# Optimization experiments

Hardware: AMD Instinct MI355X
Metric: run time of the kernel (lower is better)

## Reference

```python
import jax, jax.numpy as jnp
import numpy as np

T, G, D = 64, 1024, 128      # timesteps, detections per timestep, feature dim
N = T * G                    # total points; output rows = 3 + D = 131 cols


def setup_inputs() -> dict:
    key = jax.random.key(0)
    k1, k2 = jax.random.split(key)
    # time column: T distinct timestamps, G detections each (already time-sorted)
    times = jnp.repeat(jnp.arange(T, dtype=jnp.float32), G)
    xy = jax.random.uniform(k1, (N, 2), dtype=jnp.float32) * 128.0
    coor = jnp.concatenate([times[:, None], xy], axis=1)          # [N, 3]
    features = jax.random.normal(k2, (N, D), dtype=jnp.float32)   # [N, 128]
    return {"coor": coor, "features": features, "min_length": 8}


def _traverse(nxt):
    """Greedy chain building with a visited set (faithful to the torch loop).
    nxt[i] = precomputed best cosine match of point i in the next time group
    (-1 if i is in the last group). Returns (out_nodes, cid, clen):
      out_nodes[p] = node emitted at output slot p (all N slots filled),
      cid[p]       = chain id of slot p,
      clen[c]      = length of chain c.
    """
    def chain_cond(carry):
        visited, out, cid, p, cur, length, c = carry
        nx = nxt[cur]
        return (nx >= 0) & (~visited[nx])

    def chain_body(carry):
        visited, out, cid, p, cur, length, c = carry
        nx = nxt[cur]
        visited = visited.at[nx].set(True)
        out = out.at[p].set(nx)
        cid = cid.at[p].set(c)
        return (visited, out, cid, p + 1, nx, length + 1, c)

    def start_chain(st, start):
        visited, out, cid, clen, p, c = st
        visited = visited.at[start].set(True)
        out = out.at[p].set(start)
        cid = cid.at[p].set(c)
        carry = (visited, out, cid, p + 1, start, jnp.int32(1), c)
        visited, out, cid, p, cur, length, _ = jax.lax.while_loop(
            chain_cond, chain_body, carry)
        clen = clen.at[c].set(length)
        return (visited, out, cid, clen, p, c + 1)

    def body(start, st):
        start = jnp.int32(start)
        return jax.lax.cond(st[0][start], lambda s: s,
                            lambda s: start_chain(s, start), st)

    init = (jnp.zeros(N, bool),
            jnp.full(N, -1, jnp.int32),
            jnp.zeros(N, jnp.int32),
            jnp.zeros(N, jnp.int32),
            jnp.int32(0), jnp.int32(0))
    visited, out, cid, clen, p, c = jax.lax.fori_loop(0, N, body, init)
    return out, cid, clen


def reference(coor, features, min_length):
    # sort all points by time (stable; input is already time-sorted)
    order = jnp.argsort(coor[:, 0], stable=True)
    coor = coor[order]
    features = features[order]

    # --- vectorized precompute of the greedy next-match graph ---
    # group points by timestamp: [T, G, D]
    f = features.reshape(T, G, D)
    fn = f / jnp.maximum(jnp.linalg.norm(f, axis=-1, keepdims=True), 1e-6)
    # cosine sims between each time group and the next one: [T-1, G, G]
    sims = jnp.einsum('tgd,thd->tgh', fn[:-1], fn[1:])
    best = jnp.argmax(sims, axis=-1).astype(jnp.int32)        # [T-1, G]
    nxt = jnp.concatenate([
        (jnp.arange(1, T, dtype=jnp.int32)[:, None] * G + best).reshape(-1),
        jnp.full((G,), -1, jnp.int32)])                        # [N]
    nxt = jax.lax.stop_gradient(nxt)

    # --- sequential greedy traversal with visited set ---
    out_nodes, cid, clen = _traverse(nxt)

    # rows = [coor || features] in trajectory order
    rows = jnp.concatenate([coor, features], axis=1)[out_nodes]  # [N, 3+D]
    keep = clen[cid] >= min_length
    # pack kept rows to the top (order preserved), zero-pad the rest
    perm = jnp.argsort(~keep, stable=True)
    return jnp.where(keep[perm][:, None], rows[perm], 0.0)       # [N, 131]
```

## Files before the change

kernel.cpp:

```cpp
#include <hip/hip_runtime.h>
#include <hip/hip_bf16.h>
#include <hip/hip_fp16.h>

#define TT 64
#define GN 1024
#define DK 128
#define NN (TT * GN)
#define OUTC 131
#define TAU 5e-3f

typedef _Float16 f16x8 __attribute__((ext_vector_type(8)));
typedef float    f32x4 __attribute__((ext_vector_type(4)));

__device__ __forceinline__ unsigned f2h(float f) {
    return (unsigned)__half_as_ushort(__float2half(f));
}

__device__ __forceinline__ unsigned hup(float x) {
    __half h = __float2half(x);
    unsigned short b = __half_as_ushort(h);
    if (__half2float(h) < x)
        b = (b & 0x8000) ? (unsigned short)(b - 1) : (unsigned short)(b + 1);
    return (unsigned)b;
}

__device__ __forceinline__ void gload_lds16(const void* g, void* l) {
    __builtin_amdgcn_global_load_lds(
        (const __attribute__((address_space(1))) unsigned int*)g,
        (__attribute__((address_space(3))) unsigned int*)l, 16, 0, 0);
}

__global__ void kconv(const float* __restrict__ feat, unsigned* __restrict__ fh,
                      float* __restrict__ rnf, double* __restrict__ rnd,
                      int* __restrict__ rcnt, int* __restrict__ clen) {
    if (blockIdx.x == 0 && threadIdx.x < 63) rcnt[threadIdx.x] = 0;
    if (blockIdx.x < 256) clen[blockIdx.x * 256 + threadIdx.x] = 0;
    int row  = blockIdx.x * 4 + (threadIdx.x >> 6);
    int lane = threadIdx.x & 63;
    const float* fr = feat + (size_t)row * DK;
    float2 v = *(const float2*)(fr + lane * 2);
    fh[(size_t)row * 64 + lane] = f2h(v.x) | (f2h(v.y) << 16);
    double s = (double)v.x * (double)v.x + (double)v.y * (double)v.y;
    #pragma unroll
    for (int off = 32; off > 0; off >>= 1)
        s += __shfl_down(s, off);
    if (lane == 0) {
        double m = sqrt(s);
        if (m < 1e-6) m = 1e-6;
        double r = 1.0 / m;
        rnd[row] = r;
        rnf[row] = (float)r;
    }
}

__global__ __launch_bounds__(512) void ksim(const unsigned* __restrict__ fh,
                                            const float* __restrict__ rnf,
                                            unsigned short* __restrict__ nxt16,
                                            int* __restrict__ rcnt,
                                            int* __restrict__ rlistT,
                                            uint2* __restrict__ skt) {
    __shared__ int Tiles[8][4096];
    __shared__ float mv1[512];
    __shared__ float mv2[512];
    __shared__ int   mi1[512];

    int id = (blockIdx.x & 7) * 63 + (blockIdx.x >> 3);
    int t  = id >> 3;
    int mt = id & 7;

    int tid  = threadIdx.x;
    int wave = tid >> 6;
    int lane = tid & 63;
    int la = lane & 15;
    int lq = lane >> 4;
    int wr = (wave & 1) * 64;
    int cg = wave >> 1;
    int wc = cg * 32;

    const int* Ag = (const int*)fh + ((size_t)t * GN + mt * 128) * 64;
    const int* Bg = (const int*)fh + (size_t)(t + 1) * GN * 64;
    int* myT = &Tiles[wave][0];

    #define STAGE_Q(ntb, b)                                                  \
        {                                                                    \
            const int* Bq = Bg + ((ntb) * 128 + cg * 32) * 64;               \
            _Pragma("unroll")                                                \
            for (int i = 0; i < 8; ++i) {                                    \
                int gidx = i * 64 + lane;                                    \
                int row = gidx >> 4, colG = (gidx & 15) ^ (row & 7);         \
                gload_lds16(Bq + row * 64 + colG * 4,                        \
                            myT + (b) * 2048 + gidx * 4);                    \
            }                                                                \
        }

    STAGE_Q(0, 0)

    const float* rB = rnf + (size_t)(t + 1) * GN;

    f32x4 rnv[8][2];
    #pragma unroll
    for (int ntb = 0; ntb < 8; ++ntb)
        #pragma unroll
        for (int ct = 0; ct < 2; ++ct)
            rnv[ntb][ct] = *(const f32x4*)&rB[ntb * 128 + wc + ct * 16 + lq * 4];

    f16x8 af[4][4];
    #pragma unroll
    for (int kc = 0; kc < 4; ++kc)
        #pragma unroll
        for (int x = 0; x < 4; ++x)
            af[kc][x] = __builtin_bit_cast(f16x8,
                *(const int4*)&Ag[(wr + x * 16 + la) * 64 + (kc * 4 + lq) * 4]);

    float t1[4], t2[4]; int i1[4];
    #pragma unroll
    for (int s = 0; s < 4; ++s) { t1[s] = -3.4e38f; t2[s] = -3.4e38f; i1[s] = 0x7fffffff; }

    asm volatile("s_waitcnt vmcnt(0)" ::: "memory");

    #pragma unroll
    for (int ntb = 0; ntb < 8; ++ntb) {
        int cur = ntb & 1;
        if (ntb < 7) {
            STAGE_Q(ntb + 1, cur ^ 1)
            asm volatile("s_waitcnt vmcnt(8)" ::: "memory");
        } else {
            asm volatile("s_waitcnt vmcnt(0)" ::: "memory");
        }

        f32x4 acc[4][2];
        #pragma unroll
        for (int at = 0; at < 4; ++at)
            #pragma unroll
            for (int ct = 0; ct < 2; ++ct) acc[at][ct] = (f32x4){0.f, 0.f, 0.f, 0.f};

        const int* Bt = myT + cur * 2048;
        #pragma unroll
        for (int kc = 0; kc < 4; ++kc) {
            int sw = ((kc * 4 + lq) ^ (la & 7)) << 2;
            f16x8 bf[2];
            #pragma unroll
            for (int x = 0; x < 2; ++x)
                bf[x] = __builtin_bit_cast(f16x8, *(const int4*)&Bt[(x * 16 + la) * 64 + sw]);
            #pragma unroll
            for (int at = 0; at < 4; ++at)
                #pragma unroll
                for (int ct = 0; ct < 2; ++ct)
                    acc[at][ct] = __builtin_amdgcn_mfma_f32_16x16x32_f16(
                        bf[ct], af[kc][at], acc[at][ct], 0, 0, 0);
        }

        #pragma unroll
        for (int ct = 0; ct < 2; ++ct) {
            int nbase = ntb * 128 + wc + ct * 16 + lq * 4;
            #pragma unroll
            for (int at = 0; at < 4; ++at) {
                #pragma unroll
                for (int reg = 0; reg < 4; ++reg) {
                    float v = acc[at][ct][reg] * rnv[ntb][ct][reg];
                    t2[at] = fmaxf(t2[at], fminf(v, t1[at]));
                    if (v > t1[at]) { t1[at] = v; i1[at] = nbase + reg; }
                }
            }
        }
    }
    #undef STAGE_Q

    {
        uint2* sko = skt + (size_t)(cg * 4 + lq) * (63 * GN)
                         + (size_t)t * GN + mt * 128;
        #pragma unroll
        for (int s = 0; s < 4; ++s)
            sko[wr + s * 16 + la] = make_uint2(__float_as_uint(t1[s]),
                                               (hup(t2[s]) << 16) | (unsigned)i1[s]);
    }

    #pragma unroll
    for (int m = 16; m <= 32; m <<= 1) {
        #pragma unroll
        for (int s = 0; s < 4; ++s) {
            float o1 = __shfl_xor(t1[s], m);
            float o2 = __shfl_xor(t2[s], m);
            int   oi = __shfl_xor(i1[s], m);
            bool take = (o1 > t1[s]) || (o1 == t1[s] && oi < i1[s]);
            float nt2 = take ? fmaxf(o2, t1[s]) : fmaxf(t2[s], o1);
            if (take) { t1[s] = o1; i1[s] = oi; }
            t2[s] = nt2;
        }
    }

    if (lq == 0) {
        #pragma unroll
        for (int s = 0; s < 4; ++s) {
            int idx = (wr + s * 16 + la) * 4 + cg;
            mv1[idx] = t1[s]; mv2[idx] = t2[s]; mi1[idx] = i1[s];
        }
    }
    __syncthreads();

    if (tid < 128) {
        int r4 = tid * 4;
        float best = mv1[r4], sec = mv2[r4];
        int bi = mi1[r4];
        #pragma unroll
        for (int c = 1; c < 4; ++c) {
            float v1 = mv1[r4 + c], v2 = mv2[r4 + c];
            int  ii = mi1[r4 + c];
            if (v1 > best || (v1 == best && ii < bi)) {
                sec = fmaxf(sec, fmaxf(best, v2)); best = v1; bi = ii;
            } else {
                sec = fmaxf(sec, v1);
            }
        }
        int grow = mt * 128 + tid;
        if (best - sec < TAU) {
            int p = atomicAdd(&rcnt[t], 1);
            rlistT[t * 1024 + p] = grow;
        } else {
            nxt16[t * GN + grow] = (unsigned short)bi;
        }
    }
}

__global__ __launch_bounds__(256) void krescue(const float* __restrict__ feat,
                                               const double* __restrict__ rnd,
                                               const int* __restrict__ rcnt,
                                               const int* __restrict__ rlistT,
                                               const uint2* __restrict__ skt,
                                               unsigned short* __restrict__ nxt16) {
    int bid = blockIdx.x;
    int t = bid >> 3;
    int nr = rcnt[t];
    if (nr == 0) return;
    int tid  = threadIdx.x;
    int wave = tid >> 6, lane = tid & 63;
    int wk = (bid & 7) * 4 + wave;
    int g  = lane >> 2;
    int o  = (lane & 3) * 32;

    const float*  Bt = feat + (size_t)(t + 1) * GN * DK;
    const double* rb = rnd + (size_t)(t + 1) * GN;

    for (int ri = wk; ri < nr; ri += 32) {
        int arow = rlistT[t * 1024 + ri];

        const float* ar = feat + ((size_t)t * GN + arow) * DK + o;
        double av[32];
        #pragma unroll
        for (int j = 0; j < 32; j += 4) {
            float4 a4 = *(const float4*)(ar + j);
            av[j] = a4.x; av[j + 1] = a4.y; av[j + 2] = a4.z; av[j + 3] = a4.w;
        }

        size_t gb = (size_t)t * GN + arow;
        uint2 eg = skt[(size_t)g * (63 * GN) + gb];
        float t1  = __uint_as_float(eg.x);
        float t2u = __half2float(__ushort_as_half((unsigned short)(eg.y >> 16)));
        int   ic  = (int)(eg.y & 1023u);

        float best = t1;
        best = fmaxf(best, __shfl_xor(best, 4));
        best = fmaxf(best, __shfl_xor(best, 8));
        best = fmaxf(best, __shfl_xor(best, 16));
        best = fmaxf(best, __shfl_xor(best, 32));
        float thr = best - TAU;

        double bv = -1.0e300; int bi = 0x7fffffff;

        {
            int c = (t1 >= thr) ? ic : -1;
            double d = 0.0;
            if (c >= 0) {
                const float* br = Bt + (size_t)c * DK + o;
                #pragma unroll
                for (int jj = 0; jj < 32; jj += 4) {
                    float4 b4 = *(const float4*)(br + jj);
                    d = fma(av[jj],     (double)b4.x, d);
                    d = fma(av[jj + 1], (double)b4.y, d);
                    d = fma(av[jj + 2], (double)b4.z, d);
                    d = fma(av[jj + 3], (double)b4.w, d);
                }
            }
            d += __shfl_xor(d, 1); d += __shfl_xor(d, 2);
            if (c >= 0) {
                double v = d * rb[c];
                if (v > bv || (v == bv && c < bi)) { bv = v; bi = c; }
            }
        }

        #pragma unroll 1
        for (int s = 0; s < 16; ++s) {
            float ey = __shfl(t2u, s * 4);
            if (!(ey >= thr)) continue;
            int cgs = s >> 2, lqs = s & 3;
            #pragma unroll 1
            for (int r = 0; r < 4; ++r) {
                int j = r * 16 + g;
                int c = (j >> 3) * 128 + cgs * 32 + ((j >> 2) & 1) * 16
                      + lqs * 4 + (j & 3);
                const float* br = Bt + (size_t)c * DK + o;
                double d = 0.0;
                #pragma unroll
                for (int jj = 0; jj < 32; jj += 4) {
                    float4 b4 = *(const float4*)(br + jj);
                    d = fma(av[jj],     (double)b4.x, d);
                    d = fma(av[jj + 1], (double)b4.y, d);
                    d = fma(av[jj + 2], (double)b4.z, d);
                    d = fma(av[jj + 3], (double)b4.w, d);
                }
                d += __shfl_xor(d, 1); d += __shfl_xor(d, 2);
                double v = d * rb[c];
                if (v > bv || (v == bv && c < bi)) { bv = v; bi = c; }
            }
        }

        #pragma unroll
        for (int m = 4; m <= 32; m <<= 1) {
            double ov = __shfl_xor(bv, m);
            int    oi = __shfl_xor(bi, m);
            if (ov > bv || (ov == bv && oi < bi)) { bv = ov; bi = oi; }
        }

        if (lane == 0) nxt16[t * GN + arow] = (unsigned short)bi;
    }
}

__global__ __launch_bounds__(1024) void kgraph(const unsigned short* __restrict__ nxt16,
                                               int* __restrict__ chain_of) {
    __shared__ unsigned short ns[64 * 1024];
    __shared__ int winner[2 * GN];
    int g = threadIdx.x;

    #pragma unroll
    for (int i = 0; i < 8; ++i)
        gload_lds16((const char*)nxt16 + ((size_t)i * 1024 + g) * 16,
                    (char*)ns + ((size_t)i * 1024 + g) * 16);

    winner[g] = 0x7fffffff;
    winner[GN + g] = 0x7fffffff;
    chain_of[g] = g;
    __syncthreads();

    int mychain = g;
    for (int t = 0; t < TT - 1; ++t) {
        int* Wa = winner + (t & 1) * GN;
        int j = ns[t * GN + g];
        atomicMin(&Wa[j], mychain);
        __syncthreads();
        int w = Wa[g];
        Wa[g] = 0x7fffffff;
        mychain = (w == 0x7fffffff) ? (((t + 1) << 10) | g) : w;
        ns[t * GN + g] = (unsigned short)mychain;
    }

    for (int t = 0; t < TT - 1; ++t)
        chain_of[(t + 1) * GN + g] = ns[t * GN + g];
}

__global__ void kclen(const int* __restrict__ chain_of, int* __restrict__ clen) {
    int i = blockIdx.x * 256 + threadIdx.x;
    atomicAdd(&clen[chain_of[i]], 1);
}

__global__ __launch_bounds__(1024) void kseg(const int* __restrict__ chain_of,
                                             const int* __restrict__ clen,
                                             const int* __restrict__ minp,
                                             int* __restrict__ oloc,
                                             int* __restrict__ partial) {
    __shared__ int ps[1024];
    int b = blockIdx.x, tid = threadIdx.x;
    int i = b * 1024 + tid;
    int ml = *minp;
    int cl = clen[i];
    int v = (chain_of[i] == i && cl >= ml) ? cl : 0;
    ps[tid] = v;
    __syncthreads();
    for (int off = 1; off < 1024; off <<= 1) {
        int add = (tid >= off) ? ps[tid - off] : 0;
        __syncthreads();
        ps[tid] += add;
        __syncthreads();
    }
    oloc[i] = ps[tid] - v;
    if (tid == 1023) partial[b] = ps[tid];
}

__global__ __launch_bounds__(256) void kout(const float* __restrict__ coor,
                                            const float* __restrict__ feat,
                                            const int* __restrict__ chain_of,
                                            const int* __restrict__ clen,
                                            const int* __restrict__ oloc,
                                            const int* __restrict__ partial,
                                            const int* __restrict__ minp,
                                            float* __restrict__ out) {
    __shared__ int pb[64];
    __shared__ int stot;
    int tid = threadIdx.x;
    if (tid < 64) {
        int v = partial[tid];
        int acc = v;
        #pragma unroll
        for (int off = 1; off < 64; off <<= 1) {
            int o = __shfl_up(acc, off);
            if (tid >= off) acc += o;
        }
        pb[tid] = acc - v;
        if (tid == 63) stot = acc;
    }
    __syncthreads();

    int node = blockIdx.x * 4 + (tid >> 6);
    int lane = tid & 63;
    int s = chain_of[node];
    if (clen[s] >= *minp) {
        int row = oloc[s] + pb[s >> 10] + (node >> 10) - (s >> 10);
        float* orow = out + (size_t)row * OUTC;
        const float* f = feat + (size_t)node * DK;
        if (lane < 3) orow[lane] = coor[(size_t)node * 3 + lane];
        orow[3 + lane]  = f[lane];
        orow[67 + lane] = f[64 + lane];
    }

    int zrow = stot + blockIdx.x * 4 + (tid >> 6);
    if (zrow < NN) {
        float* orow = out + (size_t)zrow * OUTC;
        orow[lane] = 0.f;
        orow[64 + lane] = 0.f;
        if (lane < 3) orow[128 + lane] = 0.f;
    }
}

extern "C" void kernel_launch(void* const* d_in, const int* in_sizes, int n_in,
                              void* d_out, int out_size, void* d_ws, size_t ws_size,
                              hipStream_t stream) {
    const float* coor   = (const float*)d_in[0];
    const float* feat   = (const float*)d_in[1];
    const int*   minlen = (const int*)d_in[2];
    float*       out    = (float*)d_out;

    char* ws = (char*)d_ws;
    double*         rnd      = (double*)(ws);
    float*          rnf      = (float*)(ws + 524288);
    unsigned short* nxt16    = (unsigned short*)(ws + 786432);
    int*            chain_of = (int*)(ws + 917504);
    int*            clen     = (int*)(ws + 1179648);
    int*            oloc     = (int*)(ws + 1441792);
    int*            rcnt     = (int*)(ws + 1703936);
    int*            partial  = (int*)(ws + 1704192);
    int*            rlistT   = (int*)(ws + 1705216);
    unsigned*       fh       = (unsigned*)(ws + 2097152);
    uint2*          skt      = (uint2*)(ws + 18874368);

    kconv<<<NN / 4, 256, 0, stream>>>(feat, fh, rnf, rnd, rcnt, clen);

    ksim<<<63 * 8, 512, 0, stream>>>(fh, rnf, nxt16, rcnt, rlistT, skt);

    krescue<<<63 * 8, 256, 0, stream>>>(feat, rnd, rcnt, rlistT, skt, nxt16);

    kgraph<<<1, GN, 0, stream>>>(nxt16, chain_of);
    kclen<<<NN / 256, 256, 0, stream>>>(chain_of, clen);
    kseg<<<64, 1024, 0, stream>>>(chain_of, clen, minlen, oloc, partial);
    kout<<<NN / 4, 256, 0, stream>>>(coor, feat, chain_of, clen, oloc, partial,
                                     minlen, out);
}
```

Baseline: 188.5 us.

## Double ksim block to 1024 threads with 16 waves over narrower column slices

The similarity kernel now runs 1024 threads per block with 16 waves, each covering 16 columns instead of 32 per 128-column tile. This halves per-wave accumulator and B-tile work and gives more waves to hide latency. Reciprocal norms are staged once into LDS instead of being held in registers. The skt partial top-2 layout grows from 16 to 32 slices, so the rescue kernel reads two entries per row and scans 32 slices, which adds cross-wave reduction and rescue overhead.

Result: slower. 244.3 us (+29.6%).

```diff
diff --git a/kernel.cpp b/kernel.cpp
--- a/kernel.cpp
+++ b/kernel.cpp
@@ -53,16 +53,17 @@
     }
 }
 
-__global__ __launch_bounds__(512) void ksim(const unsigned* __restrict__ fh,
-                                            const float* __restrict__ rnf,
-                                            unsigned short* __restrict__ nxt16,
-                                            int* __restrict__ rcnt,
-                                            int* __restrict__ rlistT,
-                                            uint2* __restrict__ skt) {
-    __shared__ int Tiles[8][4096];
-    __shared__ float mv1[512];
-    __shared__ float mv2[512];
-    __shared__ int   mi1[512];
+__global__ __launch_bounds__(1024, 4) void ksim(const unsigned* __restrict__ fh,
+                                                const float* __restrict__ rnf,
+                                                unsigned short* __restrict__ nxt16,
+                                                int* __restrict__ rcnt,
+                                                int* __restrict__ rlistT,
+                                                uint2* __restrict__ skt) {
+    __shared__ int   Tiles[16][2048];
+    __shared__ float rnS[1024];
+    __shared__ float mv1[1024];
+    __shared__ float mv2[1024];
+    __shared__ int   mi1[1024];
 
     int id = (blockIdx.x & 7) * 63 + (blockIdx.x >> 3);
     int t  = id >> 3;
@@ -75,7 +76,7 @@
     int lq = lane >> 4;
     int wr = (wave & 1) * 64;
     int cg = wave >> 1;
-    int wc = cg * 32;
+    int wc = cg * 16;
 
     const int* Ag = (const int*)fh + ((size_t)t * GN + mt * 128) * 64;
     const int* Bg = (const int*)fh + (size_t)(t + 1) * GN * 64;
@@ -83,26 +84,21 @@
 
     #define STAGE_Q(ntb, b)                                                  \
         {                                                                    \
-            const int* Bq = Bg + ((ntb) * 128 + cg * 32) * 64;               \
+            const int* Bq = Bg + ((ntb) * 128 + cg * 16) * 64;               \
             _Pragma("unroll")                                                \
-            for (int i = 0; i < 8; ++i) {                                    \
+            for (int i = 0; i < 4; ++i) {                                    \
                 int gidx = i * 64 + lane;                                    \
                 int row = gidx >> 4, colG = (gidx & 15) ^ (row & 7);         \
                 gload_lds16(Bq + row * 64 + colG * 4,                        \
-                            myT + (b) * 2048 + gidx * 4);                    \
+                            myT + (b) * 1024 + gidx * 4);                    \
             }                                                                \
         }
 
     STAGE_Q(0, 0)
 
     const float* rB = rnf + (size_t)(t + 1) * GN;
-
-    f32x4 rnv[8][2];
-    #pragma unroll
-    for (int ntb = 0; ntb < 8; ++ntb)
-        #pragma unroll
-        for (int ct = 0; ct < 2; ++ct)
-            rnv[ntb][ct] = *(const f32x4*)&rB[ntb * 128 + wc + ct * 16 + lq * 4];
+    if (wave < 4)
+        gload_lds16(rB + wave * 256 + lane * 4, &rnS[wave * 256 + lane * 4]);
 
     f16x8 af[4][4];
     #pragma unroll
@@ -117,50 +113,42 @@
     for (int s = 0; s < 4; ++s) { t1[s] = -3.4e38f; t2[s] = -3.4e38f; i1[s] = 0x7fffffff; }
 
     asm volatile("s_waitcnt vmcnt(0)" ::: "memory");
+    __syncthreads();
 
     #pragma unroll
     for (int ntb = 0; ntb < 8; ++ntb) {
         int cur = ntb & 1;
         if (ntb < 7) {
             STAGE_Q(ntb + 1, cur ^ 1)
-            asm volatile("s_waitcnt vmcnt(8)" ::: "memory");
+            asm volatile("s_waitcnt vmcnt(4)" ::: "memory");
         } else {
             asm volatile("s_waitcnt vmcnt(0)" ::: "memory");
         }
 
-        f32x4 acc[4][2];
-        #pragma unroll
-        for (int at = 0; at < 4; ++at)
-            #pragma unroll
-            for (int ct = 0; ct < 2; ++ct) acc[at][ct] = (f32x4){0.f, 0.f, 0.f, 0.f};
-
-        const int* Bt = myT + cur * 2048;
+        f32x4 acc[4];
+        #pragma unroll
+        for (int at = 0; at < 4; ++at) acc[at] = (f32x4){0.f, 0.f, 0.f, 0.f};
+
+        const int* Bt = myT + cur * 1024;
         #pragma unroll
         for (int kc = 0; kc < 4; ++kc) {
             int sw = ((kc * 4 + lq) ^ (la & 7)) << 2;
-            f16x8 bf[2];
-            #pragma unroll
-            for (int x = 0; x < 2; ++x)
-                bf[x] = __builtin_bit_cast(f16x8, *(const int4*)&Bt[(x * 16 + la) * 64 + sw]);
+            f16x8 bf = __builtin_bit_cast(f16x8, *(const int4*)&Bt[la * 64 + sw]);
             #pragma unroll
             for (int at = 0; at < 4; ++at)
-                #pragma unroll
-                for (int ct = 0; ct < 2; ++ct)
-                    acc[at][ct] = __builtin_amdgcn_mfma_f32_16x16x32_f16(
-                        bf[ct], af[kc][at], acc[at][ct], 0, 0, 0);
-        }
-
-        #pragma unroll
-        for (int ct = 0; ct < 2; ++ct) {
-            int nbase = ntb * 128 + wc + ct * 16 + lq * 4;
+                acc[at] = __builtin_amdgcn_mfma_f32_16x16x32_f16(
+                    bf, af[kc][at], acc[at], 0, 0, 0);
+        }
+
+        f32x4 rn4 = *(const f32x4*)&rnS[ntb * 128 + wc + lq * 4];
+        int nbase = ntb * 128 + wc + lq * 4;
+        #pragma unroll
+        for (int at = 0; at < 4; ++at) {
             #pragma unroll
-            for (int at = 0; at < 4; ++at) {
-                #pragma unroll
-                for (int reg = 0; reg < 4; ++reg) {
-                    float v = acc[at][ct][reg] * rnv[ntb][ct][reg];
-                    t2[at] = fmaxf(t2[at], fminf(v, t1[at]));
-                    if (v > t1[at]) { t1[at] = v; i1[at] = nbase + reg; }
-                }
+            for (int reg = 0; reg < 4; ++reg) {
+                float v = acc[at][reg] * rn4[reg];
+                t2[at] = fmaxf(t2[at], fminf(v, t1[at]));
+                if (v > t1[at]) { t1[at] = v; i1[at] = nbase + reg; }
             }
         }
     }
@@ -192,20 +180,20 @@
     if (lq == 0) {
         #pragma unroll
         for (int s = 0; s < 4; ++s) {
-            int idx = (wr + s * 16 + la) * 4 + cg;
+            int idx = (wr + s * 16 + la) * 8 + cg;
             mv1[idx] = t1[s]; mv2[idx] = t2[s]; mi1[idx] = i1[s];
         }
     }
     __syncthreads();
 
     if (tid < 128) {
-        int r4 = tid * 4;
-        float best = mv1[r4], sec = mv2[r4];
-        int bi = mi1[r4];
-        #pragma unroll
-        for (int c = 1; c < 4; ++c) {
-            float v1 = mv1[r4 + c], v2 = mv2[r4 + c];
-            int  ii = mi1[r4 + c];
+        int r8 = tid * 8;
+        float best = mv1[r8], sec = mv2[r8];
+        int bi = mi1[r8];
+        #pragma unroll
+        for (int c = 1; c < 8; ++c) {
+            float v1 = mv1[r8 + c], v2 = mv2[r8 + c];
+            int  ii = mi1[r8 + c];
             if (v1 > best || (v1 == best && ii < bi)) {
                 sec = fmaxf(sec, fmaxf(best, v2)); best = v1; bi = ii;
             } else {
@@ -253,12 +241,16 @@
         }
 
         size_t gb = (size_t)t * GN + arow;
-        uint2 eg = skt[(size_t)g * (63 * GN) + gb];
-        float t1  = __uint_as_float(eg.x);
-        float t2u = __half2float(__ushort_as_half((unsigned short)(eg.y >> 16)));
-        int   ic  = (int)(eg.y & 1023u);
-
-        float best = t1;
+        uint2 e0 = skt[(size_t)g * (63 * GN) + gb];
+        uint2 e1 = skt[(size_t)(g + 16) * (63 * GN) + gb];
+        float t10  = __uint_as_float(e0.x);
+        float t11  = __uint_as_float(e1.x);
+        float t2u0 = __half2float(__ushort_as_half((unsigned short)(e0.y >> 16)));
+        float t2u1 = __half2float(__ushort_as_half((unsigned short)(e1.y >> 16)));
+        int   ic0  = (int)(e0.y & 1023u);
+        int   ic1  = (int)(e1.y & 1023u);
+
+        float best = fmaxf(t10, t11);
         best = fmaxf(best, __shfl_xor(best, 4));
         best = fmaxf(best, __shfl_xor(best, 8));
         best = fmaxf(best, __shfl_xor(best, 16));
@@ -267,8 +259,9 @@
 
         double bv = -1.0e300; int bi = 0x7fffffff;
 
-        {
-            int c = (t1 >= thr) ? ic : -1;
+        #pragma unroll
+        for (int h = 0; h < 2; ++h) {
+            int c = (h ? (t11 >= thr) : (t10 >= thr)) ? (h ? ic1 : ic0) : -1;
             double d = 0.0;
             if (c >= 0) {
                 const float* br = Bt + (size_t)c * DK + o;
@@ -289,15 +282,14 @@
         }
 
         #pragma unroll 1
-        for (int s = 0; s < 16; ++s) {
-            float ey = __shfl(t2u, s * 4);
+        for (int s = 0; s < 32; ++s) {
+            float ey = __shfl((s < 16) ? t2u0 : t2u1, (s & 15) * 4);
             if (!(ey >= thr)) continue;
-            int cgs = s >> 2, lqs = s & 3;
+            int scg = s >> 2, slq = s & 3;
             #pragma unroll 1
-            for (int r = 0; r < 4; ++r) {
+            for (int r = 0; r < 2; ++r) {
                 int j = r * 16 + g;
-                int c = (j >> 3) * 128 + cgs * 32 + ((j >> 2) & 1) * 16
-                      + lqs * 4 + (j & 3);
+                int c = (j >> 2) * 128 + scg * 16 + slq * 4 + (j & 3);
                 const float* br = Bt + (size_t)c * DK + o;
                 double d = 0.0;
                 #pragma unroll
@@ -453,7 +445,7 @@
 
     kconv<<<NN / 4, 256, 0, stream>>>(feat, fh, rnf, rnd, rcnt, clen);
 
-    ksim<<<63 * 8, 512, 0, stream>>>(fh, rnf, nxt16, rcnt, rlistT, skt);
+    ksim<<<63 * 8, 1024, 0, stream>>>(fh, rnf, nxt16, rcnt, rlistT, skt);
 
     krescue<<<63 * 8, 256, 0, stream>>>(feat, rnd, rcnt, rlistT, skt, nxt16);
 
```
